# Kernel optimization log

Measured on AMD Instinct MI355X. Metric: run time of the kernel, lower is better.

Reference implementation:

```python
import jax, jax.numpy as jnp
import numpy as np

DIM = 256
B = 8
H = 56
W = 56
K = 2
EPS = 1e-5  # torch BatchNorm2d default eps


def _conv1x1(x, w, b):
    # x: [B,C,H,W], w: [O,C], b: [O]
    return jnp.einsum('oc,bchw->bohw', w, x) + b[None, :, None, None]


def _bn(x, g, be, m, v):
    # inference-mode BatchNorm2d with running stats
    s = g / jnp.sqrt(v + EPS)
    return x * s[None, :, None, None] + (be - m * s)[None, :, None, None]


def _grapher(x, w1, b1, g1, be1, m1, v1, wg, bg, gg, beg, mg, vg, w2, b2, g2, be2, m2, v2):
    # fc1: 1x1 conv + BN
    h = _bn(_conv1x1(x, w1, b1), g1, be1, m1, v1)
    Hh, Ww = h.shape[2], h.shape[3]
    # MRConv4d: running max over circular-shift differences
    # torch.cat([x[:,:,-i:,:], x[:,:,:-i,:]], dim=2) == jnp.roll(x, i, axis=2)
    xj = jnp.zeros_like(h)

    def body_h(c, i):
        return jnp.maximum(c, h - jnp.roll(h, i, axis=2)), None

    xj, _ = jax.lax.scan(body_h, xj, jnp.arange(K, Hh, K))

    def body_w(c, i):
        return jnp.maximum(c, h - jnp.roll(h, i, axis=3)), None

    xj, _ = jax.lax.scan(body_w, xj, jnp.arange(K, Ww, K))

    cat = jnp.concatenate([h, xj], axis=1)  # [B, 2*dim, H, W]
    # MRConv4d.nn: Conv2d(2*dim, 2*dim, 1) -> BN(2*dim) -> GELU (exact erf)
    g = jax.nn.gelu(_bn(_conv1x1(cat, wg, bg), gg, beg, mg, vg), approximate=False)
    # fc2: Conv2d(2*dim, dim, 1) + BN(dim), then residual
    return _bn(_conv1x1(g, w2, b2), g2, be2, m2, v2) + x


def setup_inputs() -> dict:
    key = jax.random.key(0)
    ks = jax.random.split(key, 12)
    d, d2 = DIM, 2 * DIM

    def w(k, o, c):
        return jax.random.normal(k, (o, c), jnp.float32) * np.float32(1.0 / np.sqrt(c))

    return {
        'x': jax.random.normal(ks[0], (B, d, H, W), jnp.float32),
        'w1': w(ks[1], d, d), 'b1': jnp.zeros((d,), jnp.float32),
        'g1': jnp.ones((d,), jnp.float32), 'be1': jnp.zeros((d,), jnp.float32),
        'm1': jax.random.normal(ks[2], (d,), jnp.float32) * 0.1,
        'v1': jax.random.uniform(ks[3], (d,), jnp.float32, 0.5, 1.5),
        'wg': w(ks[4], d2, d2), 'bg': jnp.zeros((d2,), jnp.float32),
        'gg': jnp.ones((d2,), jnp.float32), 'beg': jnp.zeros((d2,), jnp.float32),
        'mg': jax.random.normal(ks[5], (d2,), jnp.float32) * 0.1,
        'vg': jax.random.uniform(ks[6], (d2,), jnp.float32, 0.5, 1.5),
        'w2': w(ks[7], d, d2), 'b2': jnp.zeros((d,), jnp.float32),
        'g2': jnp.ones((d,), jnp.float32), 'be2': jnp.zeros((d,), jnp.float32),
        'm2': jax.random.normal(ks[8], (d,), jnp.float32) * 0.1,
        'v2': jax.random.uniform(ks[9], (d,), jnp.float32, 0.5, 1.5),
    }


def reference(x, w1, b1, g1, be1, m1, v1, wg, bg, gg, beg, mg, vg, w2, b2, g2, be2, m2, v2):
    return _grapher(x, w1, b1, g1, be1, m1, v1, wg, bg, gg, beg, mg, vg, w2, b2, g2, be2, m2, v2)
```

## Files before the change

kernel.cpp:

```cpp
#include <hip/hip_runtime.h>
#include <math.h>

#define SPB 3136
#define NB 8
#define MTOT (NB*SPB)
#define EPS 1e-5f
#define XT_LD  288
#define CAT_LD 544

typedef unsigned short u16;
typedef __attribute__((ext_vector_type(8))) short short8;
typedef __attribute__((ext_vector_type(4))) float float4v;

__device__ __forceinline__ float b2f(u16 v){ unsigned u=((unsigned)v)<<16; float f; __builtin_memcpy(&f,&u,4); return f; }
__device__ __forceinline__ u16 f2b(float f){ unsigned u; __builtin_memcpy(&u,&f,4); u += 0x7fffu + ((u>>16)&1u); return (u16)(u>>16); }
__device__ __forceinline__ float gelu_f(float z){
  float t = 1.5957691216f * z * (1.0f + 0.044715f*z*z);
  return __fdividef(z, 1.0f + __expf(-t));
}

__device__ __forceinline__ void gll16(const u16* g, u16* l){
  __builtin_amdgcn_global_load_lds((const __attribute__((address_space(1))) void*)g,
                                   (__attribute__((address_space(3))) void*)l, 16, 0, 0);
}

__global__ void prep_k(const float* __restrict__ x, u16* __restrict__ xt,
                       const float* __restrict__ w1,const float* __restrict__ wg,const float* __restrict__ w2,
                       const float* b1,const float* g1,const float* be1,const float* m1,const float* v1,
                       const float* bg,const float* gg,const float* beg,const float* mg,const float* vg,
                       const float* b2,const float* g2,const float* be2,const float* m2,const float* v2,
                       u16* __restrict__ w1b,u16* __restrict__ wgb,u16* __restrict__ w2b,float* cst){
  __shared__ float t[32][33];
  if (blockIdx.z < 8) {
    int b = blockIdx.z, ct = blockIdx.y, st = blockIdx.x;
    int ts = threadIdx.x, tc = threadIdx.y;
    #pragma unroll
    for (int i=0;i<4;i++){
      int c = tc + i*8;
      t[c][ts] = x[((size_t)(b*256 + ct*32 + c))*SPB + st*32 + ts];
    }
    __syncthreads();
    #pragma unroll
    for (int i=0;i<4;i++){
      int r = tc + i*8;
      xt[((size_t)(b*SPB + st*32 + r))*XT_LD + ct*32 + ts] = f2b(t[ts][r]);
    }
  } else {
    int tid = threadIdx.y*32 + threadIdx.x;
    int w = ((blockIdx.z-8)*8 + blockIdx.y)*98 + blockIdx.x;
    int i = w*256 + tid;
    if (i < 65536)  w1b[(i>>8)*XT_LD  + (i&255)] = f2b(w1[i]);
    if (i < 262144) wgb[(i>>9)*CAT_LD + (i&511)] = f2b(wg[i]);
    if (i < 131072) w2b[(i>>9)*CAT_LD + (i&511)] = f2b(w2[i]);
    if (i < 256) {
      float s = g1[i]*rsqrtf(v1[i]+EPS);
      cst[i] = s; cst[256+i] = b1[i]*s + be1[i] - m1[i]*s;
      float s2 = g2[i]*rsqrtf(v2[i]+EPS);
      cst[1536+i] = s2; cst[1792+i] = b2[i]*s2 + be2[i] - m2[i]*s2;
    }
    if (i < 512) {
      float s = gg[i]*rsqrtf(vg[i]+EPS);
      cst[512+i] = s; cst[1024+i] = bg[i]*s + beg[i] - mg[i]*s;
    }
  }
}

__global__ __launch_bounds__(256) void minmax_k(const u16* __restrict__ cat, float* __restrict__ rmin, float* __restrict__ cmin){
  __shared__ float red[8][256];
  int b = blockIdx.x/56, i = blockIdx.x%56;
  int col = blockIdx.y;
  int slice = threadIdx.x >> 5;
  int c0 = (threadIdx.x & 31) * 8;
  const u16* base; size_t stride;
  if (!col){ base = cat + ((size_t)(b*SPB + i*56))*CAT_LD + c0; stride = CAT_LD; }
  else     { base = cat + ((size_t)(b*SPB + i))*CAT_LD + c0;    stride = (size_t)56*CAT_LD; }
  float m[8];
  #pragma unroll
  for (int k=0;k<8;k++) m[k]=3.4e38f;
  #pragma unroll
  for (int jj=0;jj<7;jj++){
    short8 v = *(const short8*)(base + (size_t)(slice + jj*8)*stride);
    #pragma unroll
    for (int k=0;k<8;k++) m[k] = fminf(m[k], b2f((u16)v[k]));
  }
  #pragma unroll
  for (int k=0;k<8;k++) red[slice][c0+k] = m[k];
  __syncthreads();
  int t = threadIdx.x;
  if (t < 64){
    int par = t >> 5;
    int cc = (t & 31) * 8;
    float* out = col ? cmin : rmin;
    float* p = &out[((size_t)(b*2+par)*56 + i)*256 + cc];
    #pragma unroll
    for (int k=0;k<8;k++)
      p[k] = fminf(fminf(red[par][cc+k], red[par+2][cc+k]),
                   fminf(red[par+4][cc+k], red[par+6][cc+k]));
  }
}

__global__ __launch_bounds__(256) void xj_k(u16* __restrict__ cat, const float* __restrict__ rmin, const float* __restrict__ cmin){
  int b = blockIdx.y;
  int t = threadIdx.x;
  int s = blockIdx.x*8 + (t>>5);
  int c0 = (t&31)*8;
  int y = s/56, x = s%56;
  size_t idx = ((size_t)(b*SPB + s))*CAT_LD;
  short8 h8 = *(const short8*)&cat[idx + c0];
  const float* cp = &cmin[((size_t)(b*2+(y&1))*56 + x)*256 + c0];
  const float* rp = &rmin[((size_t)(b*2+(x&1))*56 + y)*256 + c0];
  float4v cv0 = *(const float4v*)cp, cv1 = *(const float4v*)(cp+4);
  float4v rv0 = *(const float4v*)rp, rv1 = *(const float4v*)(rp+4);
  short8 o;
  #pragma unroll
  for (int j=0;j<8;j++){
    float cm = (j<4) ? cv0[j] : cv1[j-4];
    float rm = (j<4) ? rv0[j] : rv1[j-4];
    o[j] = (short)f2b(fmaxf(0.0f, b2f((u16)h8[j]) - fminf(cm, rm)));
  }
  *(short8*)&cat[idx + 256 + c0] = o;
}

__device__ __forceinline__ int xcd_remap(int orig, int nwg){
  int q = nwg >> 3, r = nwg & 7, xc = orig & 7, rest = orig >> 3;
  int base = (xc < r) ? xc*(q+1) : r*(q+1) + (xc-r)*q;
  return base + rest;
}

template<int KTOT, int LDA, int LDB, int EPI>
__global__ __launch_bounds__(512,4) void gemm_k(
    const u16* __restrict__ Ain, const u16* __restrict__ Wt,
    const float* __restrict__ scale, const float* __restrict__ bias,
    void* __restrict__ outp, const float* __restrict__ resid)
{
  __shared__ __align__(16) u16 smem[24576];
  const int tid = threadIdx.x;
  const int nwg = gridDim.x * gridDim.y;
  const int flat = blockIdx.y * gridDim.x + blockIdx.x;
  const int s_ = xcd_remap(flat, nwg);
  const int m0 = (s_ / gridDim.y) * 128;
  const int o0 = (s_ % gridDim.y) * 128;
  const int lane = tid & 63, wid = tid >> 6;
  const int quad = lane >> 4, l16 = lane & 15;

  float4v acc[8];
  #pragma unroll
  for (int j=0;j<8;j++) acc[j] = (float4v){0.f,0.f,0.f,0.f};

  const int row = tid >> 2;
  const int q8s = ((tid & 3) ^ ((tid >> 3) & 3)) * 8;
  const u16* ga0 = Ain + ((size_t)(m0 + row))*LDA + q8s;
  const u16* gb0 = Wt  + ((size_t)(o0 + row))*LDB + q8s;
  u16* l8 = smem + tid*8;

  auto STAGE = [&](int kt, int buf){
    u16* b_ = l8 + buf*8192;
    gll16(ga0 + kt, b_);
    gll16(gb0 + kt, b_ + 4096);
  };
  const int swz = (l16 >> 1) & 3;
  auto COMPUTE = [&](int buf){
    const u16* A_ = smem + buf*8192;
    const u16* B_ = A_ + 4096;
    const int kq = (quad ^ swz) * 8;
    short8 af = *(const short8*)&A_[(wid*16 + l16)*32 + kq];
    short8 bfr[8];
    #pragma unroll
    for (int in=0;in<8;in++) bfr[in] = *(const short8*)&B_[(in*16+l16)*32 + kq];
    #pragma unroll
    for (int in=0;in<8;in++)
      acc[in] = __builtin_amdgcn_mfma_f32_16x16x32_bf16(af, bfr[in], acc[in], 0, 0, 0);
  };

  constexpr int NIT = KTOT / 32;
  STAGE(0, 0);
  STAGE(32, 1);
  #pragma unroll
  for (int t = 0; t < NIT; ++t) {
    __builtin_amdgcn_sched_barrier(0);
    if (t + 1 < NIT) asm volatile("s_waitcnt vmcnt(2) lgkmcnt(0)" ::: "memory");
    else             asm volatile("s_waitcnt vmcnt(0) lgkmcnt(0)" ::: "memory");
    __builtin_amdgcn_s_barrier();
    __builtin_amdgcn_sched_barrier(0);
    if (t + 2 < NIT) STAGE((t+2)*32, (t+2)%3);
    COMPUTE(t%3);
  }
  __syncthreads();

  if (EPI == 1 || EPI == 2) {
    u16* tile = smem;
    #pragma unroll
    for (int in=0;in<8;in++){
      int ol = in*16 + l16;
      float sc = scale[o0+ol], bi = bias[o0+ol];
      #pragma unroll
      for (int r=0;r<4;r++){
        float v = acc[in][r]*sc + bi;
        if (EPI==2) v = gelu_f(v);
        tile[(wid*16+quad*4+r)*128 + ol] = f2b(v);
      }
    }
    __syncthreads();
    u16* op = (u16*)outp;
    #pragma unroll
    for (int p=0;p<4;p++){
      int chunk = p*512 + tid;
      int rr = chunk >> 4, off = (chunk & 15)*8;
      *(uint4*)&op[((size_t)(m0 + rr))*CAT_LD + o0 + off] = *(const uint4*)&tile[rr*128 + off];
    }
  } else {
    float* ftile = (float*)smem;
    float* op = (float*)outp;
    #pragma unroll
    for (int h=0; h<2; h++){
      #pragma unroll
      for (int in4=0;in4<4;in4++){
        int in = h*4 + in4;
        int c64 = in4*16 + l16;
        int og = o0 + h*64 + c64;
        float sc = scale[og], bi = bias[og];
        float4v v;
        #pragma unroll
        for (int r=0;r<4;r++) v[r] = acc[in][r]*sc + bi;
        *(float4v*)&ftile[c64*132 + wid*16 + quad*4] = v;
      }
      __syncthreads();
      #pragma unroll
      for (int p=0;p<4;p++){
        int chunk = p*512 + tid;
        int rr = chunk >> 5, off = (chunk & 31)*4;
        int m = m0 + off;
        int b = m / SPB, s = m - b*SPB;
        size_t g = ((size_t)(b*256 + o0 + h*64 + rr))*SPB + s;
        float4v v = *(const float4v*)&ftile[rr*132 + off];
        v.x += resid[g]; v.y += resid[g+1]; v.z += resid[g+2]; v.w += resid[g+3];
        *(float4v*)&op[g] = v;
      }
      __syncthreads();
    }
  }
}

extern "C" void kernel_launch(void* const* d_in, const int* in_sizes, int n_in,
                              void* d_out, int out_size, void* d_ws, size_t ws_size,
                              hipStream_t stream)
{
  const float* x  = (const float*)d_in[0];
  const float* w1 = (const float*)d_in[1];
  const float* b1 = (const float*)d_in[2];
  const float* g1 = (const float*)d_in[3];
  const float* be1= (const float*)d_in[4];
  const float* m1 = (const float*)d_in[5];
  const float* v1 = (const float*)d_in[6];
  const float* wg = (const float*)d_in[7];
  const float* bg = (const float*)d_in[8];
  const float* gg = (const float*)d_in[9];
  const float* beg= (const float*)d_in[10];
  const float* mg = (const float*)d_in[11];
  const float* vg = (const float*)d_in[12];
  const float* w2 = (const float*)d_in[13];
  const float* b2 = (const float*)d_in[14];
  const float* g2 = (const float*)d_in[15];
  const float* be2= (const float*)d_in[16];
  const float* m2 = (const float*)d_in[17];
  const float* v2 = (const float*)d_in[18];

  char* ws = (char*)d_ws;
  size_t off = 0;
  auto alloc = [&](size_t bytes){ void* p = ws + off; off += (bytes + 255) & ~(size_t)255; return p; };
  u16* xt    = (u16*)alloc((size_t)MTOT*XT_LD*2);
  u16* catt  = (u16*)alloc((size_t)MTOT*CAT_LD*2);
  u16* gt    = (u16*)alloc((size_t)MTOT*CAT_LD*2);
  u16* w1b   = (u16*)alloc((size_t)256*XT_LD*2);
  u16* wgb   = (u16*)alloc((size_t)512*CAT_LD*2);
  u16* w2b   = (u16*)alloc((size_t)256*CAT_LD*2);
  float* cst = (float*)alloc((size_t)2048*4);
  float* rmin= (float*)alloc((size_t)NB*2*56*256*4);
  float* cmin= (float*)alloc((size_t)NB*2*56*256*4);

  hipLaunchKernelGGL(prep_k, dim3(98,8,10), dim3(32,8), 0, stream,
                     x, xt, w1,wg,w2, b1,g1,be1,m1,v1, bg,gg,beg,mg,vg, b2,g2,be2,m2,v2,
                     w1b,wgb,w2b, cst);
  hipLaunchKernelGGL((gemm_k<256,XT_LD,XT_LD,1>), dim3(196,2), dim3(512), 0, stream,
                     xt, w1b, cst+0, cst+256, (void*)catt, (const float*)nullptr);
  hipLaunchKernelGGL(minmax_k, dim3(NB*56,2), dim3(256), 0, stream, catt, rmin, cmin);
  hipLaunchKernelGGL(xj_k, dim3(392, NB), dim3(256), 0, stream, catt, rmin, cmin);
  hipLaunchKernelGGL((gemm_k<512,CAT_LD,CAT_LD,2>), dim3(196,4), dim3(512), 0, stream,
                     catt, wgb, cst+512, cst+1024, (void*)gt, (const float*)nullptr);
  hipLaunchKernelGGL((gemm_k<512,CAT_LD,CAT_LD,3>), dim3(196,2), dim3(512), 0, stream,
                     gt, w2b, cst+1536, cst+1792, d_out, x);
}
```

Baseline: 179.6 us.

## Switch GEMM to BK=64 double-buffered LDS pipeline with 8-way XOR swizzle

Changes the GEMM main loop from a K-step of 32 with a triple-buffered, two-stage-ahead prefetch to a K-step of 64 with double buffering and a one-stage-ahead prefetch. Each thread now issues four 16-byte global-to-LDS loads per stage, and the LDS swizzle widens to 8 columns. The aim is to halve the number of barriers and wait points per K and run two MFMA k-substeps between syncs. In exchange, LDS grows to 64 KB per block, which may cut occupancy at launch_bounds(512,4). The shallower prefetch and the full vmcnt(0) wait also expose more load latency.

```diff
diff --git a/kernel.cpp b/kernel.cpp
--- a/kernel.cpp
+++ b/kernel.cpp
@@ -133,7 +133,7 @@
     const float* __restrict__ scale, const float* __restrict__ bias,
     void* __restrict__ outp, const float* __restrict__ resid)
 {
-  __shared__ __align__(16) u16 smem[24576];
+  __shared__ __align__(16) u16 smem[32768];
   const int tid = threadIdx.x;
   const int nwg = gridDim.x * gridDim.y;
   const int flat = blockIdx.y * gridDim.x + blockIdx.x;
@@ -147,43 +147,48 @@
   #pragma unroll
   for (int j=0;j<8;j++) acc[j] = (float4v){0.f,0.f,0.f,0.f};
 
-  const int row = tid >> 2;
-  const int q8s = ((tid & 3) ^ ((tid >> 3) & 3)) * 8;
-  const u16* ga0 = Ain + ((size_t)(m0 + row))*LDA + q8s;
-  const u16* gb0 = Wt  + ((size_t)(o0 + row))*LDB + q8s;
+  const int row8 = tid >> 3;
+  const int gc   = ((tid & 7) ^ (row8 & 7)) * 8;
+  const u16* ga0 = Ain + ((size_t)(m0 + row8))*LDA + gc;
+  const u16* ga1 = ga0 + (size_t)64*LDA;
+  const u16* gb0 = Wt  + ((size_t)(o0 + row8))*LDB + gc;
+  const u16* gb1 = gb0 + (size_t)64*LDB;
   u16* l8 = smem + tid*8;
 
   auto STAGE = [&](int kt, int buf){
-    u16* b_ = l8 + buf*8192;
+    u16* b_ = l8 + buf*16384;
     gll16(ga0 + kt, b_);
-    gll16(gb0 + kt, b_ + 4096);
+    gll16(ga1 + kt, b_ + 4096);
+    gll16(gb0 + kt, b_ + 8192);
+    gll16(gb1 + kt, b_ + 12288);
   };
-  const int swz = (l16 >> 1) & 3;
+  const int r7 = l16 & 7;
   auto COMPUTE = [&](int buf){
-    const u16* A_ = smem + buf*8192;
-    const u16* B_ = A_ + 4096;
-    const int kq = (quad ^ swz) * 8;
-    short8 af = *(const short8*)&A_[(wid*16 + l16)*32 + kq];
-    short8 bfr[8];
-    #pragma unroll
-    for (int in=0;in<8;in++) bfr[in] = *(const short8*)&B_[(in*16+l16)*32 + kq];
-    #pragma unroll
-    for (int in=0;in<8;in++)
-      acc[in] = __builtin_amdgcn_mfma_f32_16x16x32_bf16(af, bfr[in], acc[in], 0, 0, 0);
+    const u16* A_ = smem + buf*16384;
+    const u16* B_ = A_ + 8192;
+    #pragma unroll
+    for (int kk=0; kk<2; kk++){
+      const int sl = ((kk*4 + quad) ^ r7) * 8;
+      short8 af = *(const short8*)&A_[(wid*16 + l16)*64 + sl];
+      short8 bfr[8];
+      #pragma unroll
+      for (int in=0;in<8;in++) bfr[in] = *(const short8*)&B_[(in*16+l16)*64 + sl];
+      #pragma unroll
+      for (int in=0;in<8;in++)
+        acc[in] = __builtin_amdgcn_mfma_f32_16x16x32_bf16(af, bfr[in], acc[in], 0, 0, 0);
+    }
   };
 
-  constexpr int NIT = KTOT / 32;
+  constexpr int NIT = KTOT / 64;
   STAGE(0, 0);
-  STAGE(32, 1);
   #pragma unroll
   for (int t = 0; t < NIT; ++t) {
     __builtin_amdgcn_sched_barrier(0);
-    if (t + 1 < NIT) asm volatile("s_waitcnt vmcnt(2) lgkmcnt(0)" ::: "memory");
-    else             asm volatile("s_waitcnt vmcnt(0) lgkmcnt(0)" ::: "memory");
+    asm volatile("s_waitcnt vmcnt(0) lgkmcnt(0)" ::: "memory");
     __builtin_amdgcn_s_barrier();
     __builtin_amdgcn_sched_barrier(0);
-    if (t + 2 < NIT) STAGE((t+2)*32, (t+2)%3);
-    COMPUTE(t%3);
+    if (t + 1 < NIT) STAGE((t+1)*64, (t+1)&1);
+    COMPUTE(t&1);
   }
   __syncthreads();
 
```

Result: no change. 177.1 us (median of 3 runs) (-1.4%).
